# Optimization experiments

Hardware: AMD Instinct MI355X
Metric: run time of the kernel (lower is better)

## Reference

```python
import jax, jax.numpy as jnp
import numpy as np

H = W = 32
V = 1.5  # gaussian sigma used by the original _gussin(1.5)

def _gaussian_table():
    # gus[p, x, y] with p = i*32 + k, matching the original nested loops.
    r = np.arange(H, dtype=np.float64)
    d = (r[:, None, None, None] - r[None, None, :, None]) ** 2 \
        + (r[None, :, None, None] - r[None, None, None, :]) ** 2  # [i,k,x,y]
    g = np.exp(-d / (2.0 * V * V)) / (2.0 * np.pi * V * V)
    g = g.reshape(H * W, H, W)
    g = g / g.sum(axis=(1, 2), keepdims=True)  # per-position boundary normalization
    return jnp.asarray(g, dtype=jnp.float32)

_GUS = _gaussian_table()  # [1024, 32, 32]

def setup_inputs() -> dict:
    key = jax.random.key(0)
    ks = jax.random.split(key, 5)
    c, r = 1024, 16
    return {
        "x": jax.random.normal(ks[0], (1, c, H, W), jnp.float32),
        "se_w1": jax.random.normal(ks[1], (c // r, c), jnp.float32) * 0.03,
        "se_b1": jnp.zeros((c // r,), jnp.float32),
        "se_w2": jax.random.normal(ks[2], (c, c // r), jnp.float32) * 0.1,
        "se_b2": jnp.zeros((c,), jnp.float32),
        "conv_w": jax.random.normal(ks[3], (c, 2 * c), jnp.float32) * 0.02,
        "bn_gamma": jnp.ones((c,), jnp.float32),
        "bn_beta": jnp.zeros((c,), jnp.float32),
        "bn_mean": jnp.zeros((c,), jnp.float32),
        "bn_var": jnp.ones((c,), jnp.float32),
    }

def reference(x, se_w1, se_b1, se_w2, se_b2, conv_w, bn_gamma, bn_beta, bn_mean, bn_var):
    b, c, h, w = x.shape  # b == 1, h == w == 32 (hardcoded by the gaussian table)
    # ---- SE block ----
    y = x.mean(axis=(2, 3))                              # [b, c]
    y = jax.nn.relu(y @ se_w1.T + se_b1)                 # [b, c//r]
    y = jax.nn.sigmoid(y @ se_w2.T + se_b2)              # [b, c]
    x = x * y[:, :, None, None]
    # ---- gaussian spatial pooling (algebraic form of the O(H^2 W^2 C) expand) ----
    # x_spatial[c, p] = sum_{h,w} x[c,h,w] * gus[p,h,w]
    x_spatial = jnp.einsum('chw,phw->cp', x[0], _GUS).reshape(c, h, w)
    # ---- 3x3 local softmax attention on sigmoid features ----
    xr = jax.nn.sigmoid(x)                               # [1, c, h, w]
    xp = jnp.pad(xr, ((0, 0), (0, 0), (1, 1), (1, 1)))
    # torch F.unfold ordering: feature index = c_idx*9 + kh*3 + kw
    patches = jnp.stack([xp[:, :, i:i + h, j:j + w]
                         for i in range(3) for j in range(3)], axis=2)  # [1, c, 9, h, w]
    u = patches.reshape(c * 9, h * w).T                  # [hw, c*9]
    # faithful to the original reshape(hw, 3, 3, c) (reinterprets the c*9 layout)
    x3 = u.reshape(h * w, 3, 3, c)
    x1 = xr[0].transpose(1, 2, 0).reshape(h * w, 1, 1, c)
    logits = (x1 * x3).sum(-1).reshape(h * w, 9)         # [hw, 9]
    attn = jax.nn.softmax(logits, axis=1).reshape(h * w, 3, 3)
    x_range = jnp.einsum('pij,pijc->cp', attn, x3).reshape(c, h, w)
    # ---- fuse: 1x1 conv (no bias) + eval-mode BatchNorm + ReLU ----
    cat = jnp.concatenate([x_range, x_spatial], axis=0).reshape(b, 2 * c, h, w)
    out = jnp.einsum('oc,bchw->bohw', conv_w, cat)
    inv = jax.lax.rsqrt(bn_var + 1e-5)
    out = (out - bn_mean[None, :, None, None]) * (inv * bn_gamma)[None, :, None, None] \
          + bn_beta[None, :, None, None]
    return jax.nn.relu(out)
```

## Files before the change

### kernel.cpp

```cpp
#include <hip/hip_runtime.h>
#include <hip/hip_bf16.h>


typedef __attribute__((ext_vector_type(8))) short v8s;
typedef __attribute__((ext_vector_type(4))) float v4f;

__device__ __forceinline__ float sigmoidf_(float v) {
    return 1.f / (1.f + __expf(-v));
}
__device__ __forceinline__ unsigned short f2bf(float f) {
    unsigned u = __float_as_uint(f);
    u += 0x7fffu + ((u >> 16) & 1u);
    return (unsigned short)(u >> 16);
}
__device__ __forceinline__ float bf2f(unsigned short s) {
    return __uint_as_float(((unsigned)s) << 16);
}

__global__ __launch_bounds__(256) void k_mean(const float* __restrict__ x,
                                              float* __restrict__ mean) {
    int c = blockIdx.x;
    int tid = threadIdx.x;
    const float* xp = x + (size_t)c * 1024;
    float s = xp[tid] + xp[tid + 256] + xp[tid + 512] + xp[tid + 768];
    #pragma unroll
    for (int o = 32; o; o >>= 1) s += __shfl_down(s, o);
    __shared__ float wsum[4];
    if ((tid & 63) == 0) wsum[tid >> 6] = s;
    __syncthreads();
    if (tid == 0) mean[c] = (wsum[0] + wsum[1] + wsum[2] + wsum[3]) * (1.f / 1024.f);
}

__global__ __launch_bounds__(256) void k_se(const float* __restrict__ mean,
                                            const float* __restrict__ w1,
                                            const float* __restrict__ b1,
                                            const float* __restrict__ w2,
                                            const float* __restrict__ b2,
                                            float* __restrict__ y2) {
    __shared__ float ms[1024];
    __shared__ float y1[64];
    __shared__ float w2t[64 * 65];
    int tid = threadIdx.x;
    int c0 = blockIdx.x << 6;
    #pragma unroll
    for (int i = 0; i < 4; ++i) ms[tid + (i << 8)] = mean[tid + (i << 8)];
    #pragma unroll
    for (int i = 0; i < 16; ++i) {
        int idx = tid + (i << 8);
        w2t[(idx >> 6) * 65 + (idx & 63)] = w2[(size_t)c0 * 64 + idx];
    }
    __syncthreads();
    int wv = tid >> 6, lane = tid & 63;
    for (int jj = 0; jj < 16; ++jj) {
        int j = wv * 16 + jj;
        float s = 0.f;
        #pragma unroll
        for (int kk = 0; kk < 4; ++kk) {
            float4 wv4 = *(const float4*)(w1 + (size_t)j * 1024 + kk * 256 + (lane << 2));
            float4 mv  = *(const float4*)&ms[kk * 256 + (lane << 2)];
            s += wv4.x * mv.x + wv4.y * mv.y + wv4.z * mv.z + wv4.w * mv.w;
        }
        #pragma unroll
        for (int o = 32; o; o >>= 1) s += __shfl_down(s, o);
        if (lane == 0) y1[j] = fmaxf(s + b1[j], 0.f);
    }
    __syncthreads();
    if (tid < 64) {
        int c = c0 + tid;
        float s = 0.f;
        #pragma unroll 16
        for (int jj = 0; jj < 64; ++jj) s += y1[jj] * w2t[tid * 65 + jj];
        y2[c] = sigmoidf_(s + b2[c]);
    }
}

__global__ __launch_bounds__(256) void k_prep(const float* __restrict__ x,
                                              const float* __restrict__ y2,
                                              unsigned short* __restrict__ Xsb,
                                              unsigned short* __restrict__ xrb) {
    __shared__ float T[64][65];
    int tid = threadIdx.x;
    int p0 = blockIdx.x << 6, c0 = blockIdx.y << 6;
    #pragma unroll
    for (int i = 0; i < 4; ++i) {
        int idx = tid + (i << 8);
        int row = idx >> 4;
        int col = (idx & 15) << 2;
        float sc = y2[c0 + row];
        float4 v = *(const float4*)(x + (size_t)(c0 + row) * 1024 + p0 + col);
        uint2 pk;
        pk.x = (unsigned)f2bf(v.x * sc) | ((unsigned)f2bf(v.y * sc) << 16);
        pk.y = (unsigned)f2bf(v.z * sc) | ((unsigned)f2bf(v.w * sc) << 16);
        *(uint2*)(Xsb + (size_t)(c0 + row) * 1024 + p0 + col) = pk;
        T[col + 0][row] = sigmoidf_(v.x * sc);
        T[col + 1][row] = sigmoidf_(v.y * sc);
        T[col + 2][row] = sigmoidf_(v.z * sc);
        T[col + 3][row] = sigmoidf_(v.w * sc);
    }
    __syncthreads();
    #pragma unroll
    for (int i = 0; i < 4; ++i) {
        int idx = tid + (i << 8);
        int prow = idx >> 4;
        int cc = (idx & 15) << 2;
        uint2 pk;
        pk.x = (unsigned)f2bf(T[prow][cc + 0]) | ((unsigned)f2bf(T[prow][cc + 1]) << 16);
        pk.y = (unsigned)f2bf(T[prow][cc + 2]) | ((unsigned)f2bf(T[prow][cc + 3]) << 16);
        *(uint2*)(xrb + (size_t)(p0 + prow) * 1024 + c0 + cc) = pk;
    }
}

__global__ __launch_bounds__(256) void k_attn(const unsigned short* __restrict__ xrb,
                                              unsigned short* __restrict__ Bt) {
    __shared__ unsigned short val[9216];
    __shared__ float part[9][4];
    int p = blockIdx.x;
    int h = p >> 5, w = p & 31;
    int tid = threadIdx.x;
    int wv = tid >> 6, lane = tid & 63;
    #pragma unroll
    for (int rem = 0; rem < 9; ++rem) {
        int dh = rem / 3 - 1, dw = rem % 3 - 1;
        bool ok = ((unsigned)(h + dh) < 32u) && ((unsigned)(w + dw) < 32u);
        const unsigned short* rp = xrb + (size_t)((h + dh) * 32 + (w + dw)) * 1024;
        #pragma unroll
        for (int j = 0; j < 4; ++j) {
            int cf = tid + (j << 8);
            val[cf * 9 + rem] = ok ? rp[cf] : (unsigned short)0;
        }
    }
    __syncthreads();
    float ctr[4], vv[9][4], lg[9];
    #pragma unroll
    for (int j = 0; j < 4; ++j) ctr[j] = bf2f(val[(4 * tid + j) * 9 + 4]);
    #pragma unroll
    for (int q = 0; q < 9; ++q) {
        uint2 pk = *(const uint2*)&val[q * 1024 + 4 * tid];
        vv[q][0] = bf2f((unsigned short)(pk.x & 0xffffu));
        vv[q][1] = bf2f((unsigned short)(pk.x >> 16));
        vv[q][2] = bf2f((unsigned short)(pk.y & 0xffffu));
        vv[q][3] = bf2f((unsigned short)(pk.y >> 16));
        lg[q] = ctr[0] * vv[q][0] + ctr[1] * vv[q][1]
              + ctr[2] * vv[q][2] + ctr[3] * vv[q][3];
    }
    #pragma unroll
    for (int q = 0; q < 9; ++q) {
        float s = lg[q];
        #pragma unroll
        for (int o = 32; o; o >>= 1) s += __shfl_down(s, o);
        if (lane == 0) part[q][wv] = s;
    }
    __syncthreads();
    float a9[9], mx = -3.4e38f;
    #pragma unroll
    for (int q = 0; q < 9; ++q) {
        a9[q] = part[q][0] + part[q][1] + part[q][2] + part[q][3];
        mx = fmaxf(mx, a9[q]);
    }
    float se = 0.f;
    #pragma unroll
    for (int q = 0; q < 9; ++q) { a9[q] = __expf(a9[q] - mx); se += a9[q]; }
    float inv = 1.f / se;
    float o4[4] = {0.f, 0.f, 0.f, 0.f};
    #pragma unroll
    for (int q = 0; q < 9; ++q) {
        float a = a9[q] * inv;
        #pragma unroll
        for (int j = 0; j < 4; ++j) o4[j] += a * vv[q][j];
    }
    uint2 pk;
    pk.x = (unsigned)f2bf(o4[0]) | ((unsigned)f2bf(o4[1]) << 16);
    pk.y = (unsigned)f2bf(o4[2]) | ((unsigned)f2bf(o4[3]) << 16);
    *(uint2*)(Bt + (size_t)p * 2048 + 4 * tid) = pk;
}

__global__ __launch_bounds__(256) void k_gemm_sp(const unsigned short* __restrict__ B,
                                                 unsigned short* __restrict__ Bt) {
    __shared__ unsigned short As[64 * 72];
    __shared__ unsigned short Bs[64 * 72];
    __shared__ float Gs[32][32];
    int tid = threadIdx.x;
    {
        int row = tid >> 3, col0 = (tid & 7) << 2;
        float e[4], s = 0.f;
        #pragma unroll
        for (int j = 0; j < 4; ++j) {
            float d = (float)(row - (col0 + j));
            e[j] = __expf(-d * d / 4.5f);
            s += e[j];
        }
        s += __shfl_xor(s, 4, 8);
        s += __shfl_xor(s, 2, 8);
        s += __shfl_xor(s, 1, 8);
        float is = 1.f / s;
        #pragma unroll
        for (int j = 0; j < 4; ++j) Gs[row][col0 + j] = e[j] * is;
    }
    int wv = tid >> 6, lane = tid & 63;
    int wm = wv & 1, wn = wv >> 1;
    int m0 = blockIdx.y << 6, n0 = blockIdx.x << 6;
    int col = lane & 15, quad = lane >> 4;
    int sm = tid >> 2;
    int sg = (tid & 3) * 2;
    int pm = m0 + sm;
    int rr = pm >> 5, qq = pm & 31;
    v4f acc[2][2];
    #pragma unroll
    for (int i = 0; i < 2; ++i)
        #pragma unroll
        for (int j = 0; j < 2; ++j) acc[i][j] = (v4f){0.f, 0.f, 0.f, 0.f};

    const float4* pb = (const float4*)(B + (size_t)(n0 + sm) * 1024 + sg * 8);
    float4 rb0 = pb[0], rb1 = pb[1];
    for (int it = 0; it < 16; ++it) {
        __syncthreads();
        int k0 = it << 6;
        unsigned pk[8];
        #pragma unroll
        for (int jj = 0; jj < 8; ++jj) {
            int hw0 = k0 + sg * 8 + jj * 2;
            float v0 = Gs[rr][hw0 >> 5] * Gs[qq][hw0 & 31];
            float v1 = Gs[rr][(hw0 + 1) >> 5] * Gs[qq][(hw0 + 1) & 31];
            pk[jj] = (unsigned)f2bf(v0) | ((unsigned)f2bf(v1) << 16);
        }
        *(uint2*)&As[sm * 72 + sg * 8]      = *(uint2*)&pk[0];
        *(uint2*)&As[sm * 72 + sg * 8 + 4]  = *(uint2*)&pk[2];
        *(uint2*)&As[sm * 72 + sg * 8 + 8]  = *(uint2*)&pk[4];
        *(uint2*)&As[sm * 72 + sg * 8 + 12] = *(uint2*)&pk[6];
        *(float4*)&Bs[sm * 72 + sg * 8] = rb0;
        *(float4*)&Bs[sm * 72 + sg * 8 + 8] = rb1;
        __syncthreads();
        if (it + 1 < 16) {
            pb = (const float4*)(B + (size_t)(n0 + sm) * 1024 + ((it + 1) << 6) + sg * 8);
            rb0 = pb[0]; rb1 = pb[1];
        }
        #pragma unroll
        for (int ks = 0; ks < 2; ++ks) {
            int kg = ks * 4 + quad;
            int rA = wm * 32 + col;
            int rB = wn * 32 + col;
            v8s a0 = *(const v8s*)&As[rA * 72 + kg * 8];
            v8s a1 = *(const v8s*)&As[(rA + 16) * 72 + kg * 8];
            v8s b0 = *(const v8s*)&Bs[rB * 72 + kg * 8];
            v8s b1 = *(const v8s*)&Bs[(rB + 16) * 72 + kg * 8];
            acc[0][0] = __builtin_amdgcn_mfma_f32_16x16x32_bf16(a0, b0, acc[0][0], 0, 0, 0);
            acc[0][1] = __builtin_amdgcn_mfma_f32_16x16x32_bf16(a0, b1, acc[0][1], 0, 0, 0);
            acc[1][0] = __builtin_amdgcn_mfma_f32_16x16x32_bf16(a1, b0, acc[1][0], 0, 0, 0);
            acc[1][1] = __builtin_amdgcn_mfma_f32_16x16x32_bf16(a1, b1, acc[1][1], 0, 0, 0);
        }
    }
    #pragma unroll
    for (int mi = 0; mi < 2; ++mi)
        #pragma unroll
        for (int ni = 0; ni < 2; ++ni) {
            int mb = m0 + wm * 32 + mi * 16 + quad * 4;
            int nn = n0 + wn * 32 + ni * 16 + col;
            #pragma unroll
            for (int r = 0; r < 4; ++r)
                Bt[(size_t)(mb + r) * 2048 + 1024 + nn] = f2bf(acc[mi][ni][r]);
        }
}

__global__ __launch_bounds__(256) void k_packW(const float* __restrict__ W,
                                               unsigned short* __restrict__ Wb) {
    int e = (blockIdx.x * 256 + threadIdx.x) << 2;
    float4 v = *(const float4*)(W + e);
    uint2 pk;
    pk.x = (unsigned)f2bf(v.x) | ((unsigned)f2bf(v.y) << 16);
    pk.y = (unsigned)f2bf(v.z) | ((unsigned)f2bf(v.w) << 16);
    *(uint2*)(Wb + e) = pk;
}

__global__ __launch_bounds__(256) void k_gemm_main(
    const unsigned short* __restrict__ A, const unsigned short* __restrict__ B,
    float* __restrict__ outF,
    const float* __restrict__ gamma, const float* __restrict__ beta,
    const float* __restrict__ mu, const float* __restrict__ var) {
    __shared__ unsigned short As[64 * 72];
    __shared__ unsigned short Bs[64 * 72];
    const int K = 2048;
    int tid = threadIdx.x;
    int wv = tid >> 6, lane = tid & 63;
    int wm = wv & 1, wn = wv >> 1;
    int m0 = blockIdx.y << 6, n0 = blockIdx.x << 6;
    int col = lane & 15, quad = lane >> 4;
    int sm = tid >> 2;
    int sg = (tid & 3) * 2;
    v4f acc[2][2];
    #pragma unroll
    for (int i = 0; i < 2; ++i)
        #pragma unroll
        for (int j = 0; j < 2; ++j) acc[i][j] = (v4f){0.f, 0.f, 0.f, 0.f};

    const float4* pa = (const float4*)(A + (size_t)(m0 + sm) * K + sg * 8);
    const float4* pb = (const float4*)(B + (size_t)(n0 + sm) * K + sg * 8);
    float4 ra0 = pa[0], ra1 = pa[1], rb0 = pb[0], rb1 = pb[1];
    for (int it = 0; it < 32; ++it) {
        __syncthreads();
        *(float4*)&As[sm * 72 + sg * 8] = ra0;
        *(float4*)&As[sm * 72 + sg * 8 + 8] = ra1;
        *(float4*)&Bs[sm * 72 + sg * 8] = rb0;
        *(float4*)&Bs[sm * 72 + sg * 8 + 8] = rb1;
        __syncthreads();
        if (it + 1 < 32) {
            int k0 = (it + 1) << 6;
            pa = (const float4*)(A + (size_t)(m0 + sm) * K + k0 + sg * 8);
            pb = (const float4*)(B + (size_t)(n0 + sm) * K + k0 + sg * 8);
            ra0 = pa[0]; ra1 = pa[1];
            rb0 = pb[0]; rb1 = pb[1];
        }
        #pragma unroll
        for (int ks = 0; ks < 2; ++ks) {
            int kg = ks * 4 + quad;
            int rA = wm * 32 + col;
            int rB = wn * 32 + col;
            v8s a0 = *(const v8s*)&As[rA * 72 + kg * 8];
            v8s a1 = *(const v8s*)&As[(rA + 16) * 72 + kg * 8];
            v8s b0 = *(const v8s*)&Bs[rB * 72 + kg * 8];
            v8s b1 = *(const v8s*)&Bs[(rB + 16) * 72 + kg * 8];
            acc[0][0] = __builtin_amdgcn_mfma_f32_16x16x32_bf16(a0, b0, acc[0][0], 0, 0, 0);
            acc[0][1] = __builtin_amdgcn_mfma_f32_16x16x32_bf16(a0, b1, acc[0][1], 0, 0, 0);
            acc[1][0] = __builtin_amdgcn_mfma_f32_16x16x32_bf16(a1, b0, acc[1][0], 0, 0, 0);
            acc[1][1] = __builtin_amdgcn_mfma_f32_16x16x32_bf16(a1, b1, acc[1][1], 0, 0, 0);
        }
    }
    #pragma unroll
    for (int mi = 0; mi < 2; ++mi)
        #pragma unroll
        for (int ni = 0; ni < 2; ++ni) {
            int mb = m0 + wm * 32 + mi * 16 + quad * 4;
            int nn = n0 + wn * 32 + ni * 16 + col;
            #pragma unroll
            for (int r = 0; r < 4; ++r) {
                int mm = mb + r;
                float iv = rsqrtf(var[mm] + 1e-5f);
                float sc = iv * gamma[mm];
                float sh = beta[mm] - mu[mm] * sc;
                outF[((size_t)mm << 10) + nn] = fmaxf(fmaf(acc[mi][ni][r], sc, sh), 0.f);
            }
        }
}

extern "C" void kernel_launch(void* const* d_in, const int* in_sizes, int n_in,
                              void* d_out, int out_size, void* d_ws, size_t ws_size,
                              hipStream_t stream) {
    const float* x     = (const float*)d_in[0];
    const float* w1    = (const float*)d_in[1];
    const float* b1    = (const float*)d_in[2];
    const float* w2    = (const float*)d_in[3];
    const float* b2    = (const float*)d_in[4];
    const float* cw    = (const float*)d_in[5];
    const float* gamma = (const float*)d_in[6];
    const float* beta  = (const float*)d_in[7];
    const float* mu    = (const float*)d_in[8];
    const float* var   = (const float*)d_in[9];
    float* wsf = (float*)d_ws;
    unsigned short* Wb  = (unsigned short*)wsf;
    unsigned short* Bt  = (unsigned short*)(wsf + (1 << 20));
    unsigned short* Xsb = (unsigned short*)(wsf + (2 << 20));
    unsigned short* xrb = (unsigned short*)(wsf + (2 << 20) + (1 << 19));
    float* mean = wsf + (3 << 20);
    float* y2   = mean + 1024;
    float* out  = (float*)d_out;

    dim3 g16(16, 16);
    k_mean     <<<1024, 256, 0, stream>>>(x, mean);
    k_se       <<<16, 256, 0, stream>>>(mean, w1, b1, w2, b2, y2);
    k_prep     <<<g16, 256, 0, stream>>>(x, y2, Xsb, xrb);
    k_gemm_sp  <<<g16, 256, 0, stream>>>(Xsb, Bt);
    k_attn     <<<1024, 256, 0, stream>>>(xrb, Bt);
    k_packW    <<<2048, 256, 0, stream>>>(cw, Wb);
    k_gemm_main<<<g16, 256, 0, stream>>>(Wb, Bt, out, gamma, beta, mu, var);
}
```

Before: 136.9 us.

## Fuse weight packing into mean kernel and merge spatial GEMM with attention

Folds the conv-weight bf16 packing into the channel-mean kernel, widens the SE kernel to 1024 threads with a shuffle-based second matvec, and merges the gaussian spatial GEMM and local attention into a single 1280-block launch using a shared-memory union. This cuts the launch count from seven to five and lets the two independent middle stages share the GPU at the same time. The merged kernel's LDS footprint is set by the larger branch, which may lower occupancy for the attention blocks.

```diff
diff --git a/kernel.cpp b/kernel.cpp
--- a/kernel.cpp
+++ b/kernel.cpp
@@ -17,10 +17,21 @@
     return __uint_as_float(((unsigned)s) << 16);
 }
 
-__global__ __launch_bounds__(256) void k_mean(const float* __restrict__ x,
-                                              float* __restrict__ mean) {
+__global__ __launch_bounds__(256) void k_meanW(const float* __restrict__ x,
+                                               const float* __restrict__ W,
+                                               float* __restrict__ mean,
+                                               unsigned short* __restrict__ Wb) {
     int c = blockIdx.x;
     int tid = threadIdx.x;
+    size_t e0 = (size_t)c * 2048 + (size_t)tid * 8;
+    float4 v0 = *(const float4*)(W + e0);
+    float4 v1 = *(const float4*)(W + e0 + 4);
+    uint4 pk;
+    pk.x = (unsigned)f2bf(v0.x) | ((unsigned)f2bf(v0.y) << 16);
+    pk.y = (unsigned)f2bf(v0.z) | ((unsigned)f2bf(v0.w) << 16);
+    pk.z = (unsigned)f2bf(v1.x) | ((unsigned)f2bf(v1.y) << 16);
+    pk.w = (unsigned)f2bf(v1.z) | ((unsigned)f2bf(v1.w) << 16);
+    *(uint4*)(Wb + e0) = pk;
     const float* xp = x + (size_t)c * 1024;
     float s = xp[tid] + xp[tid + 256] + xp[tid + 512] + xp[tid + 768];
     #pragma unroll
@@ -31,28 +42,28 @@
     if (tid == 0) mean[c] = (wsum[0] + wsum[1] + wsum[2] + wsum[3]) * (1.f / 1024.f);
 }
 
-__global__ __launch_bounds__(256) void k_se(const float* __restrict__ mean,
-                                            const float* __restrict__ w1,
-                                            const float* __restrict__ b1,
-                                            const float* __restrict__ w2,
-                                            const float* __restrict__ b2,
-                                            float* __restrict__ y2) {
+__global__ __launch_bounds__(1024) void k_se(const float* __restrict__ mean,
+                                             const float* __restrict__ w1,
+                                             const float* __restrict__ b1,
+                                             const float* __restrict__ w2,
+                                             const float* __restrict__ b2,
+                                             float* __restrict__ y2) {
     __shared__ float ms[1024];
     __shared__ float y1[64];
     __shared__ float w2t[64 * 65];
     int tid = threadIdx.x;
     int c0 = blockIdx.x << 6;
-    #pragma unroll
-    for (int i = 0; i < 4; ++i) ms[tid + (i << 8)] = mean[tid + (i << 8)];
-    #pragma unroll
-    for (int i = 0; i < 16; ++i) {
-        int idx = tid + (i << 8);
+    ms[tid] = mean[tid];
+    #pragma unroll
+    for (int i = 0; i < 4; ++i) {
+        int idx = tid + (i << 10);
         w2t[(idx >> 6) * 65 + (idx & 63)] = w2[(size_t)c0 * 64 + idx];
     }
     __syncthreads();
     int wv = tid >> 6, lane = tid & 63;
-    for (int jj = 0; jj < 16; ++jj) {
-        int j = wv * 16 + jj;
+    #pragma unroll
+    for (int jj = 0; jj < 4; ++jj) {
+        int j = (wv << 2) + jj;
         float s = 0.f;
         #pragma unroll
         for (int kk = 0; kk < 4; ++kk) {
@@ -65,13 +76,13 @@
         if (lane == 0) y1[j] = fmaxf(s + b1[j], 0.f);
     }
     __syncthreads();
-    if (tid < 64) {
-        int c = c0 + tid;
-        float s = 0.f;
-        #pragma unroll 16
-        for (int jj = 0; jj < 64; ++jj) s += y1[jj] * w2t[tid * 65 + jj];
-        y2[c] = sigmoidf_(s + b2[c]);
-    }
+    int o = tid >> 4, l = tid & 15;
+    float s = 0.f;
+    #pragma unroll
+    for (int jj = 0; jj < 4; ++jj) s += y1[l + (jj << 4)] * w2t[o * 65 + l + (jj << 4)];
+    #pragma unroll
+    for (int o2 = 8; o2; o2 >>= 1) s += __shfl_down(s, o2, 16);
+    if (l == 0) y2[c0 + o] = sigmoidf_(s + b2[c0 + o]);
 }
 
 __global__ __launch_bounds__(256) void k_prep(const float* __restrict__ x,
@@ -110,165 +121,155 @@
     }
 }
 
-__global__ __launch_bounds__(256) void k_attn(const unsigned short* __restrict__ xrb,
-                                              unsigned short* __restrict__ Bt) {
-    __shared__ unsigned short val[9216];
-    __shared__ float part[9][4];
-    int p = blockIdx.x;
-    int h = p >> 5, w = p & 31;
-    int tid = threadIdx.x;
-    int wv = tid >> 6, lane = tid & 63;
-    #pragma unroll
-    for (int rem = 0; rem < 9; ++rem) {
-        int dh = rem / 3 - 1, dw = rem % 3 - 1;
-        bool ok = ((unsigned)(h + dh) < 32u) && ((unsigned)(w + dw) < 32u);
-        const unsigned short* rp = xrb + (size_t)((h + dh) * 32 + (w + dw)) * 1024;
-        #pragma unroll
-        for (int j = 0; j < 4; ++j) {
-            int cf = tid + (j << 8);
-            val[cf * 9 + rem] = ok ? rp[cf] : (unsigned short)0;
-        }
-    }
-    __syncthreads();
-    float ctr[4], vv[9][4], lg[9];
-    #pragma unroll
-    for (int j = 0; j < 4; ++j) ctr[j] = bf2f(val[(4 * tid + j) * 9 + 4]);
-    #pragma unroll
-    for (int q = 0; q < 9; ++q) {
-        uint2 pk = *(const uint2*)&val[q * 1024 + 4 * tid];
-        vv[q][0] = bf2f((unsigned short)(pk.x & 0xffffu));
-        vv[q][1] = bf2f((unsigned short)(pk.x >> 16));
-        vv[q][2] = bf2f((unsigned short)(pk.y & 0xffffu));
-        vv[q][3] = bf2f((unsigned short)(pk.y >> 16));
-        lg[q] = ctr[0] * vv[q][0] + ctr[1] * vv[q][1]
-              + ctr[2] * vv[q][2] + ctr[3] * vv[q][3];
-    }
-    #pragma unroll
-    for (int q = 0; q < 9; ++q) {
-        float s = lg[q];
-        #pragma unroll
-        for (int o = 32; o; o >>= 1) s += __shfl_down(s, o);
-        if (lane == 0) part[q][wv] = s;
-    }
-    __syncthreads();
-    float a9[9], mx = -3.4e38f;
-    #pragma unroll
-    for (int q = 0; q < 9; ++q) {
-        a9[q] = part[q][0] + part[q][1] + part[q][2] + part[q][3];
-        mx = fmaxf(mx, a9[q]);
-    }
-    float se = 0.f;
-    #pragma unroll
-    for (int q = 0; q < 9; ++q) { a9[q] = __expf(a9[q] - mx); se += a9[q]; }
-    float inv = 1.f / se;
-    float o4[4] = {0.f, 0.f, 0.f, 0.f};
-    #pragma unroll
-    for (int q = 0; q < 9; ++q) {
-        float a = a9[q] * inv;
-        #pragma unroll
-        for (int j = 0; j < 4; ++j) o4[j] += a * vv[q][j];
-    }
-    uint2 pk;
-    pk.x = (unsigned)f2bf(o4[0]) | ((unsigned)f2bf(o4[1]) << 16);
-    pk.y = (unsigned)f2bf(o4[2]) | ((unsigned)f2bf(o4[3]) << 16);
-    *(uint2*)(Bt + (size_t)p * 2048 + 4 * tid) = pk;
-}
-
-__global__ __launch_bounds__(256) void k_gemm_sp(const unsigned short* __restrict__ B,
-                                                 unsigned short* __restrict__ Bt) {
-    __shared__ unsigned short As[64 * 72];
-    __shared__ unsigned short Bs[64 * 72];
-    __shared__ float Gs[32][32];
-    int tid = threadIdx.x;
-    {
-        int row = tid >> 3, col0 = (tid & 7) << 2;
-        float e[4], s = 0.f;
-        #pragma unroll
-        for (int j = 0; j < 4; ++j) {
-            float d = (float)(row - (col0 + j));
-            e[j] = __expf(-d * d / 4.5f);
-            s += e[j];
-        }
-        s += __shfl_xor(s, 4, 8);
-        s += __shfl_xor(s, 2, 8);
-        s += __shfl_xor(s, 1, 8);
-        float is = 1.f / s;
-        #pragma unroll
-        for (int j = 0; j < 4; ++j) Gs[row][col0 + j] = e[j] * is;
-    }
-    int wv = tid >> 6, lane = tid & 63;
-    int wm = wv & 1, wn = wv >> 1;
-    int m0 = blockIdx.y << 6, n0 = blockIdx.x << 6;
-    int col = lane & 15, quad = lane >> 4;
-    int sm = tid >> 2;
-    int sg = (tid & 3) * 2;
-    int pm = m0 + sm;
-    int rr = pm >> 5, qq = pm & 31;
-    v4f acc[2][2];
-    #pragma unroll
-    for (int i = 0; i < 2; ++i)
-        #pragma unroll
-        for (int j = 0; j < 2; ++j) acc[i][j] = (v4f){0.f, 0.f, 0.f, 0.f};
-
-    const float4* pb = (const float4*)(B + (size_t)(n0 + sm) * 1024 + sg * 8);
-    float4 rb0 = pb[0], rb1 = pb[1];
-    for (int it = 0; it < 16; ++it) {
+union SMem {
+    struct { unsigned short As[64 * 72]; unsigned short Bs[64 * 72]; float Gs[32][32]; } sp;
+    struct { unsigned short val[9216]; float part[9][4]; } at;
+};
+
+__global__ __launch_bounds__(256) void k_spattn(const unsigned short* __restrict__ Xsb,
+                                                const unsigned short* __restrict__ xrb,
+                                                unsigned short* __restrict__ Bt) {
+    __shared__ SMem sm;
+    int tid = threadIdx.x;
+    int bx = blockIdx.x;
+    if (bx < 256) {
+        {
+            int row = tid >> 3, col0 = (tid & 7) << 2;
+            float e[4], s = 0.f;
+            #pragma unroll
+            for (int j = 0; j < 4; ++j) {
+                float d = (float)(row - (col0 + j));
+                e[j] = __expf(-d * d / 4.5f);
+                s += e[j];
+            }
+            s += __shfl_xor(s, 4, 8);
+            s += __shfl_xor(s, 2, 8);
+            s += __shfl_xor(s, 1, 8);
+            float is = 1.f / s;
+            #pragma unroll
+            for (int j = 0; j < 4; ++j) sm.sp.Gs[row][col0 + j] = e[j] * is;
+        }
+        int wv = tid >> 6, lane = tid & 63;
+        int wm = wv & 1, wn = wv >> 1;
+        int m0 = (bx >> 4) << 6, n0 = (bx & 15) << 6;
+        int col = lane & 15, quad = lane >> 4;
+        int smi = tid >> 2;
+        int sg = (tid & 3) * 2;
+        int pm = m0 + smi;
+        int rr = pm >> 5, qq = pm & 31;
+        v4f acc[2][2];
+        #pragma unroll
+        for (int i = 0; i < 2; ++i)
+            #pragma unroll
+            for (int j = 0; j < 2; ++j) acc[i][j] = (v4f){0.f, 0.f, 0.f, 0.f};
+        const float4* pb = (const float4*)(Xsb + (size_t)(n0 + smi) * 1024 + sg * 8);
+        float4 rb0 = pb[0], rb1 = pb[1];
+        for (int it = 0; it < 16; ++it) {
+            __syncthreads();
+            int k0 = it << 6;
+            unsigned pk[8];
+            #pragma unroll
+            for (int jj = 0; jj < 8; ++jj) {
+                int hw0 = k0 + sg * 8 + jj * 2;
+                float v0 = sm.sp.Gs[rr][hw0 >> 5] * sm.sp.Gs[qq][hw0 & 31];
+                float v1 = sm.sp.Gs[rr][(hw0 + 1) >> 5] * sm.sp.Gs[qq][(hw0 + 1) & 31];
+                pk[jj] = (unsigned)f2bf(v0) | ((unsigned)f2bf(v1) << 16);
+            }
+            *(uint2*)&sm.sp.As[smi * 72 + sg * 8]      = *(uint2*)&pk[0];
+            *(uint2*)&sm.sp.As[smi * 72 + sg * 8 + 4]  = *(uint2*)&pk[2];
+            *(uint2*)&sm.sp.As[smi * 72 + sg * 8 + 8]  = *(uint2*)&pk[4];
+            *(uint2*)&sm.sp.As[smi * 72 + sg * 8 + 12] = *(uint2*)&pk[6];
+            *(float4*)&sm.sp.Bs[smi * 72 + sg * 8] = rb0;
+            *(float4*)&sm.sp.Bs[smi * 72 + sg * 8 + 8] = rb1;
+            __syncthreads();
+            if (it + 1 < 16) {
+                pb = (const float4*)(Xsb + (size_t)(n0 + smi) * 1024 + ((it + 1) << 6) + sg * 8);
+                rb0 = pb[0]; rb1 = pb[1];
+            }
+            #pragma unroll
+            for (int ks = 0; ks < 2; ++ks) {
+                int kg = ks * 4 + quad;
+                int rA = wm * 32 + col;
+                int rB = wn * 32 + col;
+                v8s a0 = *(const v8s*)&sm.sp.As[rA * 72 + kg * 8];
+                v8s a1 = *(const v8s*)&sm.sp.As[(rA + 16) * 72 + kg * 8];
+                v8s b0 = *(const v8s*)&sm.sp.Bs[rB * 72 + kg * 8];
+                v8s b1 = *(const v8s*)&sm.sp.Bs[(rB + 16) * 72 + kg * 8];
+                acc[0][0] = __builtin_amdgcn_mfma_f32_16x16x32_bf16(a0, b0, acc[0][0], 0, 0, 0);
+                acc[0][1] = __builtin_amdgcn_mfma_f32_16x16x32_bf16(a0, b1, acc[0][1], 0, 0, 0);
+                acc[1][0] = __builtin_amdgcn_mfma_f32_16x16x32_bf16(a1, b0, acc[1][0], 0, 0, 0);
+                acc[1][1] = __builtin_amdgcn_mfma_f32_16x16x32_bf16(a1, b1, acc[1][1], 0, 0, 0);
+            }
+        }
+        #pragma unroll
+        for (int mi = 0; mi < 2; ++mi)
+            #pragma unroll
+            for (int ni = 0; ni < 2; ++ni) {
+                int mb = m0 + wm * 32 + mi * 16 + quad * 4;
+                int nn = n0 + wn * 32 + ni * 16 + col;
+                #pragma unroll
+                for (int r = 0; r < 4; ++r)
+                    Bt[(size_t)(mb + r) * 2048 + 1024 + nn] = f2bf(acc[mi][ni][r]);
+            }
+    } else {
+        int p = bx - 256;
+        int h = p >> 5, w = p & 31;
+        int wv = tid >> 6, lane = tid & 63;
+        #pragma unroll
+        for (int rem = 0; rem < 9; ++rem) {
+            int dh = rem / 3 - 1, dw = rem % 3 - 1;
+            bool ok = ((unsigned)(h + dh) < 32u) && ((unsigned)(w + dw) < 32u);
+            const unsigned short* rp = xrb + (size_t)((h + dh) * 32 + (w + dw)) * 1024;
+            #pragma unroll
+            for (int j = 0; j < 4; ++j) {
+                int cf = tid + (j << 8);
+                sm.at.val[cf * 9 + rem] = ok ? rp[cf] : (unsigned short)0;
+            }
+        }
         __syncthreads();
-        int k0 = it << 6;
-        unsigned pk[8];
-        #pragma unroll
-        for (int jj = 0; jj < 8; ++jj) {
-            int hw0 = k0 + sg * 8 + jj * 2;
-            float v0 = Gs[rr][hw0 >> 5] * Gs[qq][hw0 & 31];
-            float v1 = Gs[rr][(hw0 + 1) >> 5] * Gs[qq][(hw0 + 1) & 31];
-            pk[jj] = (unsigned)f2bf(v0) | ((unsigned)f2bf(v1) << 16);
-        }
-        *(uint2*)&As[sm * 72 + sg * 8]      = *(uint2*)&pk[0];
-        *(uint2*)&As[sm * 72 + sg * 8 + 4]  = *(uint2*)&pk[2];
-        *(uint2*)&As[sm * 72 + sg * 8 + 8]  = *(uint2*)&pk[4];
-        *(uint2*)&As[sm * 72 + sg * 8 + 12] = *(uint2*)&pk[6];
-        *(float4*)&Bs[sm * 72 + sg * 8] = rb0;
-        *(float4*)&Bs[sm * 72 + sg * 8 + 8] = rb1;
+        float ctr[4], vv[9][4], lg[9];
+        #pragma unroll
+        for (int j = 0; j < 4; ++j) ctr[j] = bf2f(sm.at.val[(4 * tid + j) * 9 + 4]);
+        #pragma unroll
+        for (int q = 0; q < 9; ++q) {
+            uint2 pk = *(const uint2*)&sm.at.val[q * 1024 + 4 * tid];
+            vv[q][0] = bf2f((unsigned short)(pk.x & 0xffffu));
+            vv[q][1] = bf2f((unsigned short)(pk.x >> 16));
+            vv[q][2] = bf2f((unsigned short)(pk.y & 0xffffu));
+            vv[q][3] = bf2f((unsigned short)(pk.y >> 16));
+            lg[q] = ctr[0] * vv[q][0] + ctr[1] * vv[q][1]
+                  + ctr[2] * vv[q][2] + ctr[3] * vv[q][3];
+        }
+        #pragma unroll
+        for (int q = 0; q < 9; ++q) {
+            float s = lg[q];
+            #pragma unroll
+            for (int o = 32; o; o >>= 1) s += __shfl_down(s, o);
+            if (lane == 0) sm.at.part[q][wv] = s;
+        }
         __syncthreads();
-        if (it + 1 < 16) {
-            pb = (const float4*)(B + (size_t)(n0 + sm) * 1024 + ((it + 1) << 6) + sg * 8);
-            rb0 = pb[0]; rb1 = pb[1];
-        }
-        #pragma unroll
-        for (int ks = 0; ks < 2; ++ks) {
-            int kg = ks * 4 + quad;
-            int rA = wm * 32 + col;
-            int rB = wn * 32 + col;
-            v8s a0 = *(const v8s*)&As[rA * 72 + kg * 8];
-            v8s a1 = *(const v8s*)&As[(rA + 16) * 72 + kg * 8];
-            v8s b0 = *(const v8s*)&Bs[rB * 72 + kg * 8];
-            v8s b1 = *(const v8s*)&Bs[(rB + 16) * 72 + kg * 8];
-            acc[0][0] = __builtin_amdgcn_mfma_f32_16x16x32_bf16(a0, b0, acc[0][0], 0, 0, 0);
-            acc[0][1] = __builtin_amdgcn_mfma_f32_16x16x32_bf16(a0, b1, acc[0][1], 0, 0, 0);
-            acc[1][0] = __builtin_amdgcn_mfma_f32_16x16x32_bf16(a1, b0, acc[1][0], 0, 0, 0);
-            acc[1][1] = __builtin_amdgcn_mfma_f32_16x16x32_bf16(a1, b1, acc[1][1], 0, 0, 0);
-        }
-    }
-    #pragma unroll
-    for (int mi = 0; mi < 2; ++mi)
-        #pragma unroll
-        for (int ni = 0; ni < 2; ++ni) {
-            int mb = m0 + wm * 32 + mi * 16 + quad * 4;
-            int nn = n0 + wn * 32 + ni * 16 + col;
-            #pragma unroll
-            for (int r = 0; r < 4; ++r)
-                Bt[(size_t)(mb + r) * 2048 + 1024 + nn] = f2bf(acc[mi][ni][r]);
-        }
-}
-
-__global__ __launch_bounds__(256) void k_packW(const float* __restrict__ W,
-                                               unsigned short* __restrict__ Wb) {
-    int e = (blockIdx.x * 256 + threadIdx.x) << 2;
-    float4 v = *(const float4*)(W + e);
-    uint2 pk;
-    pk.x = (unsigned)f2bf(v.x) | ((unsigned)f2bf(v.y) << 16);
-    pk.y = (unsigned)f2bf(v.z) | ((unsigned)f2bf(v.w) << 16);
-    *(uint2*)(Wb + e) = pk;
+        float a9[9], mx = -3.4e38f;
+        #pragma unroll
+        for (int q = 0; q < 9; ++q) {
+            a9[q] = sm.at.part[q][0] + sm.at.part[q][1] + sm.at.part[q][2] + sm.at.part[q][3];
+            mx = fmaxf(mx, a9[q]);
+        }
+        float se = 0.f;
+        #pragma unroll
+        for (int q = 0; q < 9; ++q) { a9[q] = __expf(a9[q] - mx); se += a9[q]; }
+        float inv = 1.f / se;
+        float o4[4] = {0.f, 0.f, 0.f, 0.f};
+        #pragma unroll
+        for (int q = 0; q < 9; ++q) {
+            float a = a9[q] * inv;
+            #pragma unroll
+            for (int j = 0; j < 4; ++j) o4[j] += a * vv[q][j];
+        }
+        uint2 pk;
+        pk.x = (unsigned)f2bf(o4[0]) | ((unsigned)f2bf(o4[1]) << 16);
+        pk.y = (unsigned)f2bf(o4[2]) | ((unsigned)f2bf(o4[3]) << 16);
+        *(uint2*)(Bt + (size_t)p * 2048 + 4 * tid) = pk;
+    }
 }
 
 __global__ __launch_bounds__(256) void k_gemm_main(
@@ -364,11 +365,9 @@
     float* out  = (float*)d_out;
 
     dim3 g16(16, 16);
-    k_mean     <<<1024, 256, 0, stream>>>(x, mean);
-    k_se       <<<16, 256, 0, stream>>>(mean, w1, b1, w2, b2, y2);
+    k_meanW    <<<1024, 256, 0, stream>>>(x, cw, mean, Wb);
+    k_se       <<<16, 1024, 0, stream>>>(mean, w1, b1, w2, b2, y2);
     k_prep     <<<g16, 256, 0, stream>>>(x, y2, Xsb, xrb);
-    k_gemm_sp  <<<g16, 256, 0, stream>>>(Xsb, Bt);
-    k_attn     <<<1024, 256, 0, stream>>>(xrb, Bt);
-    k_packW    <<<2048, 256, 0, stream>>>(cw, Wb);
+    k_spattn   <<<1280, 256, 0, stream>>>(Xsb, xrb, Bt);
     k_gemm_main<<<g16, 256, 0, stream>>>(Wb, Bt, out, gamma, beta, mu, var);
 }
```

New measurement: 134.7 us. Within noise of the previous version (-1.6%).
